# Optimization experiments

Hardware: AMD Instinct MI355X
Metric: run time of the kernel (lower is better)

## Reference

```python
import jax, jax.numpy as jnp
import numpy as np

D_MODEL = 1024
N_HEADS = 16
D_K = D_MODEL // N_HEADS


def setup_inputs() -> dict:
    key = jax.random.key(0)
    ks = jax.random.split(key, 12)
    B, S = 4, 2048
    sc = 1.0 / np.sqrt(D_MODEL)
    inp = {
        "query": jax.random.normal(ks[0], (B, S, D_MODEL), jnp.float32),
        "key": jax.random.normal(ks[1], (B, S, D_MODEL), jnp.float32),
        "value": jax.random.normal(ks[2], (B, S, D_MODEL), jnp.float32),
        "Wq": jax.random.normal(ks[3], (D_MODEL, D_MODEL), jnp.float32) * sc,
        "bq": jnp.zeros((D_MODEL,), jnp.float32),
        "Wk": jax.random.normal(ks[4], (D_MODEL, D_MODEL), jnp.float32) * sc,
        "bk": jnp.zeros((D_MODEL,), jnp.float32),
        "Wv": jax.random.normal(ks[5], (D_MODEL, D_MODEL), jnp.float32) * sc,
        "bv": jnp.zeros((D_MODEL,), jnp.float32),
        "Wo": jax.random.normal(ks[6], (D_MODEL, D_MODEL), jnp.float32) * sc,
        "bo": jnp.zeros((D_MODEL,), jnp.float32),
    }
    return inp


def _split_heads(x):
    B, S, _ = x.shape
    return x.reshape(B, S, N_HEADS, D_K).transpose(0, 2, 1, 3)  # [B,H,S,Dk]


def reference(query, key, value, Wq, bq, Wk, bk, Wv, bv, Wo, bo):
    q = _split_heads(query @ Wq.T + bq)
    k = _split_heads(key @ Wk.T + bk)
    v = _split_heads(value @ Wv.T + bv)
    scores = jnp.einsum("bhqd,bhkd->bhqk", q, k) / jnp.sqrt(jnp.float32(D_K))
    # Faithful to source: softmax over dim=1 (the HEAD axis), a quirk of the original.
    probs = jax.nn.softmax(scores, axis=1)
    attn = jnp.einsum("bhqk,bhkd->bhqd", probs, v)
    B, H, S, Dk = attn.shape
    combined = attn.transpose(0, 2, 1, 3).reshape(B, S, H * Dk)
    return combined @ Wo.T + bo
```

## Files before the change

kernel.cpp:

```cpp
#include <hip/hip_runtime.h>
#include <stdint.h>

typedef __attribute__((ext_vector_type(8))) short bf16x8;
typedef __attribute__((ext_vector_type(4))) float f32x4;
typedef __attribute__((ext_vector_type(4))) float fl4;
typedef __attribute__((ext_vector_type(4))) unsigned short u16x4;
typedef __attribute__((ext_vector_type(8))) unsigned short u16x8;
typedef __attribute__((ext_vector_type(2))) uint32_t u32x2;

constexpr int SEQ = 2048;
constexpr int DMODEL = 1024;
constexpr int NH = 16;
constexpr int DKH = 64;
constexpr float SEXP = 0.18033688f;

__device__ __forceinline__ unsigned short f2bf(float x) {
  union { float f; uint32_t u; } c;
  c.f = x;
  uint32_t u = c.u;
  u += 0x7FFFu + ((u >> 16) & 1u);
  return (unsigned short)(u >> 16);
}

__device__ __forceinline__ float bf2f(unsigned short u) {
  union { uint32_t u; float f; } c;
  c.u = ((uint32_t)u) << 16;
  return c.f;
}

__device__ __forceinline__ uint32_t cvtpk(float lo, float hi) {
  uint32_t r;
  asm("v_cvt_pk_bf16_f32 %0, %1, %2" : "=v"(r) : "v"(lo), "v"(hi));
  return r;
}

#if __has_builtin(__builtin_amdgcn_exp2f)
__device__ __forceinline__ float fexp2(float x) { return __builtin_amdgcn_exp2f(x); }
#else
__device__ __forceinline__ float fexp2(float x) { return exp2f(x); }
#endif

__device__ __forceinline__ int swz(int row) { return (row & 3) ^ ((row >> 2) & 3); }

__device__ __forceinline__ void gload16(const unsigned short* g, unsigned short* l) {
  __builtin_amdgcn_global_load_lds((const __attribute__((address_space(1))) void*)g,
                                   (__attribute__((address_space(3))) void*)l, 16, 0, 0);
}

__global__ __launch_bounds__(256) void cvtk(
    const float* __restrict__ s0, const float* __restrict__ s1, const float* __restrict__ s2,
    unsigned short* __restrict__ d0, unsigned short* __restrict__ d1, unsigned short* __restrict__ d2) {
  const float* s = blockIdx.y == 0 ? s0 : blockIdx.y == 1 ? s1 : s2;
  unsigned short* d = blockIdx.y == 0 ? d0 : blockIdx.y == 1 ? d1 : d2;
  const size_t i = ((size_t)blockIdx.x * 256 + threadIdx.x) * 8;
  fl4 a = *(const fl4*)(s + i);
  fl4 c = *(const fl4*)(s + i + 4);
  u16x8 r;
#pragma unroll
  for (int j = 0; j < 4; ++j) { r[j] = f2bf(a[j]); r[4 + j] = f2bf(c[j]); }
  *(u16x8*)(d + i) = r;
}

__global__ __launch_bounds__(256) void cvt1(
    const float* __restrict__ s, unsigned short* __restrict__ d) {
  const size_t i = ((size_t)blockIdx.x * 256 + threadIdx.x) * 8;
  fl4 a = *(const fl4*)(s + i);
  fl4 c = *(const fl4*)(s + i + 4);
  u16x8 r;
#pragma unroll
  for (int j = 0; j < 4; ++j) { r[j] = f2bf(a[j]); r[4 + j] = f2bf(c[j]); }
  *(u16x8*)(d + i) = r;
}

template <int EPI>
__global__ __launch_bounds__(256, 2) void gemm3(
    const unsigned short* __restrict__ A, const unsigned short* __restrict__ Bb,
    const float* __restrict__ bias, void* __restrict__ Cp, float ascale) {
  constexpr int K = DMODEL;
  constexpr int N = DMODEL;
  __shared__ unsigned short As[2][128 * 32];
  __shared__ unsigned short Bs[2][128 * 32];
  const int tid = threadIdx.x;
  const int wave = tid >> 6, lane = tid & 63;
  const int g = lane >> 4, ln = lane & 15;
  const int o = blockIdx.x;
  const int x = o & 7, idx = o >> 3;
  const int r0 = (x * 8 + (idx & 7)) * 128;
  const int c0 = (idx >> 3) * 128;
  const int wr = (wave >> 1) * 64, wc = (wave & 1) * 64;

  f32x4 acc[4][4] = {};

  auto STAGE = [&](int buf, int kt) {
#pragma unroll
    for (int i = 0; i < 2; ++i) {
      const int row = i * 64 + (tid >> 2);
      const int cs = ((tid & 3) ^ swz(row)) * 8;
      gload16(A + (size_t)(r0 + row) * K + kt + cs, As[buf] + (i * 256 + wave * 64) * 8);
      gload16(Bb + (size_t)(c0 + row) * K + kt + cs, Bs[buf] + (i * 256 + wave * 64) * 8);
    }
  };

  STAGE(0, 0);
  __syncthreads();

  for (int t = 0; t < K / 32; ++t) {
    const int buf = t & 1;
    if (t + 1 < K / 32) STAGE(buf ^ 1, (t + 1) * 32);
    bf16x8 af[4], bfr[4];
#pragma unroll
    for (int m = 0; m < 4; ++m) {
      const int row = wr + m * 16 + ln;
      af[m] = *(const bf16x8*)(As[buf] + row * 32 + ((g ^ swz(row)) * 8));
    }
#pragma unroll
    for (int n = 0; n < 4; ++n) {
      const int row = wc + n * 16 + ln;
      bfr[n] = *(const bf16x8*)(Bs[buf] + row * 32 + ((g ^ swz(row)) * 8));
    }
#pragma unroll
    for (int m = 0; m < 4; ++m)
#pragma unroll
      for (int n = 0; n < 4; ++n)
        acc[m][n] = __builtin_amdgcn_mfma_f32_16x16x32_bf16(af[m], bfr[n], acc[m][n], 0, 0, 0);
    __syncthreads();
  }

#pragma unroll
  for (int m = 0; m < 4; ++m) {
    const int row = r0 + wr + m * 16 + g * 4;
#pragma unroll
    for (int n = 0; n < 4; ++n) {
      const int col = c0 + wc + n * 16 + ln;
      const float bv = bias[col];
      f32x4 v = acc[m][n];
      if (EPI == 2) {
        float* C = (float*)Cp;
#pragma unroll
        for (int r = 0; r < 4; ++r) C[(size_t)(row + r) * N + col] = (v[r] + bv) * ascale;
      } else if (EPI == 0) {
        unsigned short* C = (unsigned short*)Cp;
#pragma unroll
        for (int r = 0; r < 4; ++r) C[(size_t)(row + r) * N + col] = f2bf((v[r] + bv) * ascale);
      } else {
        unsigned short* Vt = (unsigned short*)Cp;
        const int bb = row >> 11, sl = row & 2047;
        const int h = col >> 6, d = col & 63;
        u16x4 pk;
#pragma unroll
        for (int r = 0; r < 4; ++r) pk[r] = f2bf((v[r] + bv) * ascale);
        *(u16x4*)(Vt + ((size_t)((bb * NH + h) * DKH + d)) * SEQ + sl) = pk;
      }
    }
  }
}

__global__ __launch_bounds__(256, 3) void denomk(
    const unsigned short* __restrict__ Qp, const unsigned short* __restrict__ Kp,
    unsigned short* __restrict__ rDb) {
  const int tid = threadIdx.x, wave = tid >> 6, lane = tid & 63;
  const int g = lane >> 4, ln = lane & 15;
  const int o = blockIdx.x;
  const int l = (o & 7) * 256 + (o >> 3);
  const int b = l >> 9;
  const int qg = (l >> 4) & 31;
  const int kvg = l & 15;
  const int q0 = qg * 64, kv0 = kvg * 128 + wave * 32;

  f32x4 psum[2][4] = {};

  for (int h = 0; h < NH; ++h) {
    const int hb = h * DKH;
    bf16x8 qf[2][4];
#pragma unroll
    for (int ks = 0; ks < 2; ++ks)
#pragma unroll
      for (int n = 0; n < 4; ++n)
        qf[ks][n] = *(const bf16x8*)(Qp + (size_t)(b * SEQ + q0 + n * 16 + ln) * DMODEL + hb + ks * 32 + g * 8);
    bf16x8 kf[2][2];
#pragma unroll
    for (int m = 0; m < 2; ++m)
#pragma unroll
      for (int ks = 0; ks < 2; ++ks)
        kf[m][ks] = *(const bf16x8*)(Kp + (size_t)(b * SEQ + kv0 + m * 16 + ln) * DMODEL + hb + ks * 32 + g * 8);
    f32x4 s[2][4] = {};
#pragma unroll
    for (int m = 0; m < 2; ++m)
#pragma unroll
      for (int n = 0; n < 4; ++n) {
        s[m][n] = __builtin_amdgcn_mfma_f32_16x16x32_bf16(kf[m][0], qf[0][n], s[m][n], 0, 0, 0);
        s[m][n] = __builtin_amdgcn_mfma_f32_16x16x32_bf16(kf[m][1], qf[1][n], s[m][n], 0, 0, 0);
      }
#pragma unroll
    for (int m = 0; m < 2; ++m)
#pragma unroll
      for (int n = 0; n < 4; ++n)
#pragma unroll
        for (int r = 0; r < 4; ++r) psum[m][n][r] += fexp2(s[m][n][r]);
  }

#pragma unroll
  for (int m = 0; m < 2; ++m)
#pragma unroll
    for (int n = 0; n < 4; ++n) {
      u16x4 st;
#pragma unroll
      for (int r = 0; r < 4; ++r) st[r] = f2bf(1.0f / psum[m][n][r]);
      *(u16x4*)(rDb + (size_t)(b * SEQ + q0 + n * 16 + ln) * SEQ + kv0 + m * 16 + g * 4) = st;
    }
}

__global__ __launch_bounds__(256, 4) void flashk(
    const unsigned short* __restrict__ Qp, const unsigned short* __restrict__ Kp,
    const unsigned short* __restrict__ Vt, const unsigned short* __restrict__ rDb,
    unsigned short* __restrict__ Ab) {
  __shared__ unsigned short Ks[2][32 * 128];
  __shared__ unsigned short Vs[2][128 * 32];
  __shared__ unsigned short Pl[8][16 * 32];
  const int tid = threadIdx.x, wave = tid >> 6, lane = tid & 63;
  const int g = lane >> 4, ln = lane & 15;
  const int o = blockIdx.x;
  const int l = (o & 7) * 128 + (o >> 3);
  const int b = l >> 8;
  const int hp = (l >> 5) & 7;
  const int qg0 = (l & 31) * 64;
  const int hl = wave >> 1, h = hp * 2 + hl;
  const int qg = qg0 + (wave & 1) * 32;

  bf16x8 qf[2][2];
#pragma unroll
  for (int ks = 0; ks < 2; ++ks)
#pragma unroll
    for (int n = 0; n < 2; ++n)
      qf[ks][n] = *(const bf16x8*)(Qp + (size_t)(b * SEQ + qg + n * 16 + ln) * DMODEL + h * DKH + ks * 32 + g * 8);

  f32x4 ao[4][2] = {};
  const size_t rbase0 = (size_t)(b * SEQ + qg + ln) * SEQ;

  auto STAGE = [&](int buf, int kv0) {
#pragma unroll
    for (int i = 0; i < 2; ++i) {
      const int s = i * 256 + tid;
      {
        const int row = s >> 4, c = s & 15;
        gload16(Kp + (size_t)(b * SEQ + kv0 + row) * DMODEL + hp * 128 + ((c ^ (row & 7)) * 8),
                Ks[buf] + (i * 256 + wave * 64) * 8);
      }
      {
        const int row = s >> 2, c = s & 3;
        gload16(Vt + ((size_t)((b * NH + hp * 2 + (row >> 6)) * DKH + (row & 63))) * SEQ + kv0 + ((c ^ (row & 3)) * 8),
                Vs[buf] + (i * 256 + wave * 64) * 8);
      }
    }
  };

  STAGE(0, 0);
  __syncthreads();

  for (int t = 0; t < SEQ / 32; ++t) {
    const int kv0 = t * 32, buf = t & 1;
    u16x4 rdq[2][2];
#pragma unroll
    for (int n = 0; n < 2; ++n)
#pragma unroll
      for (int m = 0; m < 2; ++m)
        rdq[n][m] = *(const u16x4*)(rDb + rbase0 + (size_t)(n * 16) * SEQ + kv0 + m * 16 + g * 4);
    if (t + 1 < SEQ / 32) STAGE(buf ^ 1, kv0 + 32);

    f32x4 s2[2][2] = {};
    __builtin_amdgcn_s_setprio(1);
#pragma unroll
    for (int m = 0; m < 2; ++m) {
      const int row = m * 16 + ln;
#pragma unroll
      for (int ks = 0; ks < 2; ++ks) {
        const int c = hl * 8 + ks * 4 + g;
        bf16x8 kf = *(const bf16x8*)(Ks[buf] + row * 128 + ((c ^ (row & 7)) * 8));
#pragma unroll
        for (int n = 0; n < 2; ++n)
          s2[m][n] = __builtin_amdgcn_mfma_f32_16x16x32_bf16(kf, qf[ks][n], s2[m][n], 0, 0, 0);
      }
    }
    __builtin_amdgcn_s_setprio(0);

#pragma unroll
    for (int n = 0; n < 2; ++n) {
      unsigned short* pb = Pl[wave * 2 + n];
#pragma unroll
      for (int m = 0; m < 2; ++m) {
        float p[4];
#pragma unroll
        for (int r = 0; r < 4; ++r) p[r] = fexp2(s2[m][n][r]) * bf2f(rdq[n][m][r]);
        u32x2 wv;
        wv[0] = cvtpk(p[0], p[1]);
        wv[1] = cvtpk(p[2], p[3]);
        const int ch = (m * 2 + (g >> 1)) ^ swz(ln);
        *(u32x2*)(pb + ln * 32 + ch * 8 + (g & 1) * 4) = wv;
      }
    }
    bf16x8 pfr[2];
#pragma unroll
    for (int n = 0; n < 2; ++n)
      pfr[n] = *(const bf16x8*)(Pl[wave * 2 + n] + ln * 32 + ((g ^ swz(ln)) * 8));

    __builtin_amdgcn_s_setprio(1);
#pragma unroll
    for (int dt = 0; dt < 4; ++dt) {
      const int vrow = hl * 64 + dt * 16 + ln;
      bf16x8 vf = *(const bf16x8*)(Vs[buf] + vrow * 32 + ((g ^ (vrow & 3)) * 8));
#pragma unroll
      for (int n = 0; n < 2; ++n)
        ao[dt][n] = __builtin_amdgcn_mfma_f32_16x16x32_bf16(vf, pfr[n], ao[dt][n], 0, 0, 0);
    }
    __builtin_amdgcn_s_setprio(0);
    __syncthreads();
  }

#pragma unroll
  for (int dt = 0; dt < 4; ++dt)
#pragma unroll
    for (int n = 0; n < 2; ++n) {
      u16x4 st;
#pragma unroll
      for (int r = 0; r < 4; ++r) st[r] = f2bf(ao[dt][n][r]);
      *(u16x4*)(Ab + (size_t)(b * SEQ + qg + n * 16 + ln) * DMODEL + h * DKH + dt * 16 + g * 4) = st;
    }
}

extern "C" void kernel_launch(void* const* d_in, const int* in_sizes, int n_in,
                              void* d_out, int out_size, void* d_ws, size_t ws_size,
                              hipStream_t stream) {
  (void)in_sizes; (void)n_in; (void)out_size; (void)ws_size;
  const float* query = (const float*)d_in[0];
  const float* key   = (const float*)d_in[1];
  const float* value = (const float*)d_in[2];
  const float* Wq = (const float*)d_in[3];
  const float* bq = (const float*)d_in[4];
  const float* Wk = (const float*)d_in[5];
  const float* bk = (const float*)d_in[6];
  const float* Wv = (const float*)d_in[7];
  const float* bv = (const float*)d_in[8];
  const float* Wo = (const float*)d_in[9];
  const float* bo = (const float*)d_in[10];

  uint8_t* ws = (uint8_t*)d_ws;
  const size_t SZ = (size_t)4 * SEQ * DMODEL * 2;
  const size_t WSZ = (size_t)DMODEL * DMODEL;
  unsigned short* Xv = (unsigned short*)(ws);
  unsigned short* Qp = (unsigned short*)(ws);
  unsigned short* Wob = (unsigned short*)(ws);
  unsigned short* Kp = (unsigned short*)(ws + SZ);
  unsigned short* Vt = (unsigned short*)(ws + 2 * SZ);
  unsigned short* Ab = (unsigned short*)(ws + 3 * SZ);
  unsigned short* Wqb = Ab;
  unsigned short* Wkb = Ab + WSZ;
  unsigned short* Wvb = Ab + 2 * WSZ;
  unsigned short* Xq = (unsigned short*)d_out;
  unsigned short* Xk = (unsigned short*)d_out + (size_t)4 * SEQ * DMODEL;
  unsigned short* rDb = (unsigned short*)d_out;

  cvtk<<<dim3(4096, 3), 256, 0, stream>>>(query, key, value, Xq, Xk, Xv);
  cvtk<<<dim3(512, 3), 256, 0, stream>>>(Wq, Wk, Wv, Wqb, Wkb, Wvb);
  gemm3<1><<<512, 256, 0, stream>>>(Xv, Wvb, bv, Vt, 1.0f);
  gemm3<0><<<512, 256, 0, stream>>>(Xq, Wqb, bq, Qp, SEXP);
  gemm3<0><<<512, 256, 0, stream>>>(Xk, Wkb, bk, Kp, 1.0f);
  denomk<<<2048, 256, 0, stream>>>(Qp, Kp, rDb);
  flashk<<<1024, 256, 0, stream>>>(Qp, Kp, Vt, rDb, Ab);
  cvt1<<<512, 256, 0, stream>>>(Wo, Wob);
  gemm3<2><<<512, 256, 0, stream>>>(Ab, Wob, bo, (float*)d_out, 1.0f);
}
```

Measured before the change: 475.0 us.

## Double-buffer K tiles in shared memory for the softmax denominator kernel

The denominator kernel now stages each head's 128x64 K tile into double-buffered LDS with an XOR swizzle, using async global-to-LDS loads. The next head's tile is prefetched while the current one is consumed, instead of each wave reading K fragments directly from global memory. This aims to hide global load latency and coalesce the K loads, at the cost of 32KB of LDS per block and a barrier every head iteration, which may lower occupancy.

```diff
diff --git a/kernel.cpp b/kernel.cpp
--- a/kernel.cpp
+++ b/kernel.cpp
@@ -158,6 +158,7 @@
 __global__ __launch_bounds__(256, 3) void denomk(
     const unsigned short* __restrict__ Qp, const unsigned short* __restrict__ Kp,
     unsigned short* __restrict__ rDb) {
+  __shared__ unsigned short Ks[2][128 * 64];
   const int tid = threadIdx.x, wave = tid >> 6, lane = tid & 63;
   const int g = lane >> 4, ln = lane & 15;
   const int o = blockIdx.x;
@@ -165,24 +166,42 @@
   const int b = l >> 9;
   const int qg = (l >> 4) & 31;
   const int kvg = l & 15;
-  const int q0 = qg * 64, kv0 = kvg * 128 + wave * 32;
+  const int q0 = qg * 64, kvb = kvg * 128;
+  const int kw = wave * 32;
+
+  auto STAGE = [&](int buf, int h) {
+#pragma unroll
+    for (int i = 0; i < 4; ++i) {
+      const int s = i * 256 + tid;
+      const int row = s >> 3, c = s & 7;
+      gload16(Kp + (size_t)(b * SEQ + kvb + row) * DMODEL + h * DKH + ((c ^ (row & 7)) * 8),
+              Ks[buf] + (i * 256 + wave * 64) * 8);
+    }
+  };
 
   f32x4 psum[2][4] = {};
 
+  STAGE(0, 0);
+  __syncthreads();
+
   for (int h = 0; h < NH; ++h) {
-    const int hb = h * DKH;
+    const int buf = h & 1;
+    if (h + 1 < NH) STAGE(buf ^ 1, h + 1);
     bf16x8 qf[2][4];
 #pragma unroll
     for (int ks = 0; ks < 2; ++ks)
 #pragma unroll
       for (int n = 0; n < 4; ++n)
-        qf[ks][n] = *(const bf16x8*)(Qp + (size_t)(b * SEQ + q0 + n * 16 + ln) * DMODEL + hb + ks * 32 + g * 8);
+        qf[ks][n] = *(const bf16x8*)(Qp + (size_t)(b * SEQ + q0 + n * 16 + ln) * DMODEL + h * DKH + ks * 32 + g * 8);
     bf16x8 kf[2][2];
 #pragma unroll
     for (int m = 0; m < 2; ++m)
 #pragma unroll
-      for (int ks = 0; ks < 2; ++ks)
-        kf[m][ks] = *(const bf16x8*)(Kp + (size_t)(b * SEQ + kv0 + m * 16 + ln) * DMODEL + hb + ks * 32 + g * 8);
+      for (int ks = 0; ks < 2; ++ks) {
+        const int r = kw + m * 16 + ln;
+        const int cc = ks * 4 + g;
+        kf[m][ks] = *(const bf16x8*)(Ks[buf] + r * 64 + ((cc ^ (r & 7)) * 8));
+      }
     f32x4 s[2][4] = {};
 #pragma unroll
     for (int m = 0; m < 2; ++m)
@@ -197,6 +216,7 @@
       for (int n = 0; n < 4; ++n)
 #pragma unroll
         for (int r = 0; r < 4; ++r) psum[m][n][r] += fexp2(s[m][n][r]);
+    __syncthreads();
   }
 
 #pragma unroll
@@ -206,7 +226,7 @@
       u16x4 st;
 #pragma unroll
       for (int r = 0; r < 4; ++r) st[r] = f2bf(1.0f / psum[m][n][r]);
-      *(u16x4*)(rDb + (size_t)(b * SEQ + q0 + n * 16 + ln) * SEQ + kv0 + m * 16 + g * 4) = st;
+      *(u16x4*)(rDb + (size_t)(b * SEQ + q0 + n * 16 + ln) * SEQ + kvb + kw + m * 16 + g * 4) = st;
     }
 }
 
```

Result: faster. 437.5 us (-7.9%).
